# Kernel optimization log

Hardware: AMD Instinct MI355X
Metric: run time of the kernel (lower is better)

The kernel has to match this reference:

```python
import jax, jax.numpy as jnp
import numpy as np

HID = 768          # args.hidden_size
LSTM2 = 768        # args.lstm_dim * 2
SCALE = HID ** -0.5


def _cross_attn(q_in, kv_in, Wq, bq, Wk, bk, Wv, bv):
    # Linear projections (weights stored as [in, out])
    Q = q_in @ Wq + bq            # [B, Sq, H]
    K = kv_in @ Wk + bk           # [B, Sk, H]
    V = kv_in @ Wv + bv           # [B, Sk, H]
    attn = jnp.einsum('bqh,bkh->bqk', Q, K) * SCALE
    attn = jax.nn.softmax(attn, axis=-1)
    return jnp.einsum('bqk,bkh->bqh', attn, V)


def setup_inputs() -> dict:
    key = jax.random.key(0)
    ks = jax.random.split(key, 14)
    B, Ssyn, Ssem = 4, 4096, 2048
    syntactic_feat = jax.random.normal(ks[0], (B, Ssyn, LSTM2), jnp.float32)
    semantic_feat = jax.random.normal(ks[1], (B, Ssem, HID), jnp.float32)

    def lin(k, fan_in, fan_out):
        kw, kb = jax.random.split(k)
        bound = 1.0 / np.sqrt(fan_in)
        W = jax.random.uniform(kw, (fan_in, fan_out), jnp.float32, -bound, bound)
        b = jax.random.uniform(kb, (fan_out,), jnp.float32, -bound, bound)
        return W, b

    # syntax_to_semantic: query_dim=HID, key_dim=LSTM2
    Wq1, bq1 = lin(ks[2], HID, HID)
    Wk1, bk1 = lin(ks[3], LSTM2, HID)
    Wv1, bv1 = lin(ks[4], LSTM2, HID)
    # semantic_to_syntax: query_dim=LSTM2, key_dim=HID
    Wq2, bq2 = lin(ks[5], LSTM2, HID)
    Wk2, bk2 = lin(ks[6], HID, HID)
    Wv2, bv2 = lin(ks[7], HID, HID)
    return dict(syntactic_feat=syntactic_feat, semantic_feat=semantic_feat,
                Wq1=Wq1, bq1=bq1, Wk1=Wk1, bk1=bk1, Wv1=Wv1, bv1=bv1,
                Wq2=Wq2, bq2=bq2, Wk2=Wk2, bk2=bk2, Wv2=Wv2, bv2=bv2)


def reference(syntactic_feat, semantic_feat,
              Wq1, bq1, Wk1, bk1, Wv1, bv1,
              Wq2, bq2, Wk2, bk2, Wv2, bv2):
    # enhanced_semantic: queries from semantic, keys/values from syntactic
    enhanced_semantic = _cross_attn(semantic_feat, syntactic_feat,
                                    Wq1, bq1, Wk1, bk1, Wv1, bv1)
    # enhanced_syntax: queries from syntactic, keys/values from semantic
    enhanced_syntax = _cross_attn(syntactic_feat, semantic_feat,
                                  Wq2, bq2, Wk2, bk2, Wv2, bv2)
    return enhanced_semantic, enhanced_syntax
```

## Files before the change

kernel.cpp:

```cpp
#include <hip/hip_runtime.h>
#include <stdint.h>


typedef unsigned short u16;
typedef __attribute__((ext_vector_type(8))) __bf16 bf16x8;
typedef __attribute__((ext_vector_type(4))) float f32x4;

__device__ __forceinline__ float bf2f(u16 u) {
  union { unsigned int i; float f; } x; x.i = ((unsigned int)u) << 16; return x.f;
}
__device__ __forceinline__ u16 f2bf(float f) {
  union { float f; unsigned int i; } x; x.f = f;
  unsigned int i = x.i;
  i += 0x7fffu + ((i >> 16) & 1u);
  return (u16)(i >> 16);
}

__device__ __forceinline__ void cp16(void* lds, const void* g) {
  __builtin_amdgcn_global_load_lds((__attribute__((address_space(1))) void*)g,
                                   (__attribute__((address_space(3))) void*)lds,
                                   16, 0, 0);
}

struct GemmDesc {
  const u16* A; const u16* Bt; const float* bias; void* C;
  long sA, sB, sC;
  int K, lda, ldb, ldc;
  int gx, gy;
  int start;
  int mode, outf;
  float scale;
};
struct GemmPack { GemmDesc d[6]; int nd; };

#define PHASE(MH, I0, PAR, RDB, STAGE, WAITC)                                 \
  {                                                                           \
    const bf16x8* As8 =                                                       \
        (const bf16x8*)((const char*)L + (PAR) * 32768 + (MH) * 16384);       \
    bf16x8 a0[2][2];                                                          \
    _Pragma("unroll")                                                         \
    for (int s = 0; s < 2; ++s)                                               \
      _Pragma("unroll")                                                       \
      for (int i = 0; i < 2; ++i) a0[s][i] = As8[iaq[s][(I0) + i]];           \
    if (RDB) {                                                                \
      const bf16x8* Bl8 =                                                     \
          (const bf16x8*)((const char*)L + 65536 + (PAR) * 32768);            \
      const bf16x8* Bh8 =                                                     \
          (const bf16x8*)((const char*)L + 65536 + (PAR) * 32768 + 16384);    \
      _Pragma("unroll")                                                       \
      for (int s = 0; s < 2; ++s)                                             \
        _Pragma("unroll")                                                     \
        for (int j = 0; j < 2; ++j) {                                         \
          bfr[0][s][j] = Bl8[ibq[s][j]];                                      \
          bfr[1][s][j] = Bh8[ibq[s][j]];                                      \
        }                                                                     \
    }                                                                         \
    STAGE;                                                                    \
    if (RDB) { asm volatile("s_waitcnt lgkmcnt(8)" ::: "memory"); }           \
    __builtin_amdgcn_s_barrier();                                             \
    asm volatile("s_waitcnt lgkmcnt(0)" ::: "memory");                        \
    __builtin_amdgcn_s_setprio(1);                                            \
    _Pragma("unroll")                                                         \
    for (int s = 0; s < 2; ++s)                                               \
      _Pragma("unroll")                                                       \
      for (int i = 0; i < 2; ++i)                                             \
        _Pragma("unroll")                                                     \
        for (int nh = 0; nh < 2; ++nh)                                        \
          _Pragma("unroll")                                                   \
          for (int j = 0; j < 2; ++j)                                         \
            acc[MH][nh][(I0) + i][j] =                                        \
                __builtin_amdgcn_mfma_f32_16x16x32_bf16(                      \
                    bfr[nh][s][j], a0[s][i], acc[MH][nh][(I0) + i][j],        \
                    0, 0, 0);                                                 \
    __builtin_amdgcn_s_setprio(0);                                            \
    WAITC;                                                                    \
    __builtin_amdgcn_s_barrier();                                             \
  }

__global__ __launch_bounds__(512, 2)
void gemm256_kernel(GemmPack p)
{
  __shared__ __align__(16) u16 L[65536];

  int seg = 0;
#pragma unroll
  for (int t = 1; t < 6; ++t)
    if (t < p.nd && (int)blockIdx.x >= p.d[t].start) seg = t;
  const GemmDesc& g = p.d[seg];
  const int local = (int)blockIdx.x - g.start;
  const int pxy = g.gx * g.gy;
  const int bz = local / pxy;
  const int rem = local - bz * pxy;
  const int by = rem / g.gx;
  const int bx = rem - by * g.gx;

  const int tid  = threadIdx.x;
  const int lane = tid & 63;
  const int wave = tid >> 6;
  const int l15  = lane & 15;
  const int quad = lane >> 4;
  const int wm   = wave >> 2;
  const int wn   = wave & 3;

  const char* Ab = (const char*)(g.A + (long)bz * g.sA + (long)bx * 256 * g.lda);
  const char* Bb = (const char*)(g.Bt + (long)bz * g.sB + (long)by * 256 * g.ldb);
  const long ldaB = (long)g.lda * 2;
  const long ldbB = (long)g.ldb * 2;

  const int gchk = (lane & 7) ^ (lane >> 3);
  const char* pa0 = Ab + (long)(wave * 8 + (lane >> 3)) * ldaB + (gchk << 4);
  const char* pb0 = Bb + (long)(wave * 8 + (lane >> 3)) * ldbB + (gchk << 4);
  char* lA = (char*)L + wave * 1024;
  char* lB = (char*)L + 65536 + wave * 1024;

  auto stA = [&](int tile, int h) {
    char* d = lA + (tile & 1) * 32768 + h * 16384;
    const char* s = pa0 + (long)h * 128 * ldaB + ((long)tile << 7);
    cp16(d, s);
    cp16(d + 8192, s + 64 * ldaB);
  };
  auto stB = [&](int tile, int h) {
    char* d = lB + (tile & 1) * 32768 + h * 16384;
    const char* s = pb0 + (long)h * 128 * ldbB + ((long)tile << 7);
    cp16(d, s);
    cp16(d + 8192, s + 64 * ldbB);
  };

  int iaq[2][4], ibq[2][2];
#pragma unroll
  for (int s = 0; s < 2; ++s) {
#pragma unroll
    for (int i = 0; i < 4; ++i)
      iaq[s][i] = (wm * 64 + i * 16 + l15) * 8 + ((s * 4 + quad) ^ (l15 & 7));
#pragma unroll
    for (int j = 0; j < 2; ++j)
      ibq[s][j] = (wn * 32 + j * 16 + l15) * 8 + ((s * 4 + quad) ^ (l15 & 7));
  }

  f32x4 acc[2][2][4][2];
  {
    f32x4 zz = {0.f, 0.f, 0.f, 0.f};
#pragma unroll
    for (int mh = 0; mh < 2; ++mh)
#pragma unroll
      for (int nh = 0; nh < 2; ++nh)
#pragma unroll
        for (int i = 0; i < 4; ++i)
#pragma unroll
          for (int j = 0; j < 2; ++j) acc[mh][nh][i][j] = zz;
  }
  bf16x8 bfr[2][2][2];

  stB(0, 0); stB(0, 1); stA(0, 0); stA(0, 1);
  stB(1, 0); stB(1, 1); stA(1, 0);
  asm volatile("s_waitcnt vmcnt(6)" ::: "memory");
  __builtin_amdgcn_s_barrier();

  const int nt = g.K >> 6;
  const int NI = nt >> 1;
  for (int it = 0; it < NI; ++it) {
    const int t = it * 2;
    const bool m2 = (t + 2) < nt;
    const bool m3 = (t + 3) < nt;
    PHASE(0, 0, 0, 1, stA(t + 1, 1), )
    PHASE(0, 2, 0, 0, if (m2) stB(t + 2, 0), )
    PHASE(1, 0, 0, 0, if (m2) stB(t + 2, 1), )
    PHASE(1, 2, 0, 0, if (m2) stA(t + 2, 0),
          if (m2) { asm volatile("s_waitcnt vmcnt(6)" ::: "memory"); }
          else    { asm volatile("s_waitcnt vmcnt(0)" ::: "memory"); })
    PHASE(0, 0, 1, 1, if (m2) stA(t + 2, 1), )
    PHASE(0, 2, 1, 0, if (m3) stB(t + 3, 0), )
    PHASE(1, 0, 1, 0, if (m3) stB(t + 3, 1), )
    PHASE(1, 2, 1, 0, if (m3) stA(t + 3, 0),
          if (m3)      { asm volatile("s_waitcnt vmcnt(6)" ::: "memory"); }
          else if (m2) { asm volatile("s_waitcnt vmcnt(0)" ::: "memory"); })
  }

  const long cbase = (long)bz * g.sC;
#pragma unroll
  for (int mh = 0; mh < 2; ++mh) {
#pragma unroll
    for (int i = 0; i < 4; ++i) {
      const int row = bx * 256 + mh * 128 + wm * 64 + i * 16 + l15;
      const float rbias = (g.mode == 2) ? g.bias[row] : 0.f;
#pragma unroll
      for (int nh = 0; nh < 2; ++nh) {
#pragma unroll
        for (int j = 0; j < 2; ++j) {
          const int colbase = by * 256 + nh * 128 + wn * 32 + j * 16 + quad * 4;
          float v[4];
#pragma unroll
          for (int r = 0; r < 4; ++r) v[r] = acc[mh][nh][i][j][r] * g.scale;
          if (g.mode == 1) {
            const float4 cb = *(const float4*)(g.bias + colbase);
            v[0] += cb.x; v[1] += cb.y; v[2] += cb.z; v[3] += cb.w;
          } else if (g.mode == 2) {
#pragma unroll
            for (int r = 0; r < 4; ++r) v[r] += rbias;
          }
          const long idx = cbase + (long)row * g.ldc + colbase;
          if (g.outf) {
            float4 st; st.x = v[0]; st.y = v[1]; st.z = v[2]; st.w = v[3];
            *(float4*)((float*)g.C + idx) = st;
          } else {
            uint2 st;
            st.x = (unsigned int)f2bf(v[0]) | ((unsigned int)f2bf(v[1]) << 16);
            st.y = (unsigned int)f2bf(v[2]) | ((unsigned int)f2bf(v[3]) << 16);
            *(uint2*)((u16*)g.C + idx) = st;
          }
        }
      }
    }
  }
}

__global__ __launch_bounds__(256)
void cvt2_bf16_kernel(const float* __restrict__ sa, u16* __restrict__ da, int n8a,
                      const float* __restrict__ sb, u16* __restrict__ db, int n8b)
{
  int idx = blockIdx.x * 256 + threadIdx.x;
  const float* src; u16* dst; int i;
  if (idx < n8a) { src = sa; dst = da; i = idx; }
  else           { src = sb; dst = db; i = idx - n8a; if (i >= n8b) return; }
  const float4* s4 = (const float4*)src;
  float4 a = s4[i * 2], b = s4[i * 2 + 1];
  uint4 o;
  o.x = (unsigned int)f2bf(a.x) | ((unsigned int)f2bf(a.y) << 16);
  o.y = (unsigned int)f2bf(a.z) | ((unsigned int)f2bf(a.w) << 16);
  o.z = (unsigned int)f2bf(b.x) | ((unsigned int)f2bf(b.y) << 16);
  o.w = (unsigned int)f2bf(b.z) | ((unsigned int)f2bf(b.w) << 16);
  ((uint4*)dst)[i] = o;
}

__global__ void transpose6_kernel(const float* s0, const float* s1, const float* s2,
                                  const float* s3, const float* s4, const float* s5,
                                  u16* d0, u16* d1, u16* d2,
                                  u16* d3, u16* d4, u16* d5)
{
  __shared__ float t[32][33];
  const float* src; u16* dst;
  switch (blockIdx.z) {
    case 0: src = s0; dst = d0; break;
    case 1: src = s1; dst = d1; break;
    case 2: src = s2; dst = d2; break;
    case 3: src = s3; dst = d3; break;
    case 4: src = s4; dst = d4; break;
    default: src = s5; dst = d5; break;
  }
  const int tx = threadIdx.x, ty = threadIdx.y;
  const int x = blockIdx.x * 32 + tx;
  const int y0 = blockIdx.y * 32;
#pragma unroll
  for (int j = 0; j < 32; j += 8) t[ty + j][tx] = src[(long)(y0 + ty + j) * 768 + x];
  __syncthreads();
  const int x2 = y0 + tx;
#pragma unroll
  for (int j = 0; j < 32; j += 8)
    dst[(long)(blockIdx.x * 32 + ty + j) * 768 + x2] = f2bf(t[tx][ty + j]);
}

template <int NV>
__device__ __forceinline__ void softmax_row(u16* row)
{
  __shared__ float red[8];
  const int tid  = threadIdx.x;
  const int lane = tid & 63;
  const int wave = tid >> 6;
  uint4* p4 = (uint4*)row;

  uint4 ld[NV / 8];
#pragma unroll
  for (int c = 0; c < NV / 8; ++c) ld[c] = p4[tid + c * 256];
  float v[NV];
#pragma unroll
  for (int c = 0; c < NV / 8; ++c) {
    unsigned int w[4] = {ld[c].x, ld[c].y, ld[c].z, ld[c].w};
#pragma unroll
    for (int q = 0; q < 4; ++q) {
      v[c * 8 + q * 2]     = bf2f((u16)(w[q] & 0xffffu));
      v[c * 8 + q * 2 + 1] = bf2f((u16)(w[q] >> 16));
    }
  }

  float m = -1e30f;
#pragma unroll
  for (int i = 0; i < NV; ++i) m = fmaxf(m, v[i]);
#pragma unroll
  for (int off = 32; off > 0; off >>= 1) m = fmaxf(m, __shfl_xor(m, off, 64));
  if (lane == 0) red[wave] = m;
  __syncthreads();
  m = fmaxf(fmaxf(red[0], red[1]), fmaxf(red[2], red[3]));

  float s = 0.f;
#pragma unroll
  for (int i = 0; i < NV; ++i) { v[i] = __expf(v[i] - m); s += v[i]; }
#pragma unroll
  for (int off = 32; off > 0; off >>= 1) s += __shfl_xor(s, off, 64);
  if (lane == 0) red[4 + wave] = s;
  __syncthreads();
  s = (red[4] + red[5]) + (red[6] + red[7]);
  const float inv = 1.0f / s;

#pragma unroll
  for (int c = 0; c < NV / 8; ++c) {
    unsigned int w[4];
#pragma unroll
    for (int q = 0; q < 4; ++q) {
      const u16 lo = f2bf(v[c * 8 + q * 2] * inv);
      const u16 hi = f2bf(v[c * 8 + q * 2 + 1] * inv);
      w[q] = (unsigned int)lo | ((unsigned int)hi << 16);
    }
    uint4 st; st.x = w[0]; st.y = w[1]; st.z = w[2]; st.w = w[3];
    p4[tid + c * 256] = st;
  }
}

__global__ __launch_bounds__(256)
void softmax_both_kernel(u16* S1, u16* S2, const u16* cpy_src, u16* cpy_dst)
{
  if (blockIdx.x < 8192) { softmax_row<16>(S1 + (long)blockIdx.x * 4096); return; }
  if (blockIdx.x < 24576) { softmax_row<8>(S2 + (long)(blockIdx.x - 8192) * 2048); return; }
  const long base = (long)(blockIdx.x - 24576) * 512 + threadIdx.x;
  const uint4* s = (const uint4*)cpy_src;
  uint4* d = (uint4*)cpy_dst;
  d[base] = s[base];
  d[base + 256] = s[base + 256];
}


static GemmDesc mkdesc(const void* A, const void* Bt, const float* bias, void* C,
                       long sA, long sB, long sC, int K, int lda, int ldb, int ldc,
                       int M, int N, int start, int mode, int outf, float scale)
{
  GemmDesc d;
  d.A = (const u16*)A; d.Bt = (const u16*)Bt; d.bias = bias; d.C = C;
  d.sA = sA; d.sB = sB; d.sC = sC;
  d.K = K; d.lda = lda; d.ldb = ldb; d.ldc = ldc;
  d.gx = M / 256; d.gy = N / 256; d.start = start;
  d.mode = mode; d.outf = outf; d.scale = scale;
  return d;
}

extern "C" void kernel_launch(void* const* d_in, const int* in_sizes, int n_in,
                              void* d_out, int out_size, void* d_ws, size_t ws_size,
                              hipStream_t stream)
{
  (void)in_sizes; (void)n_in; (void)out_size; (void)ws_size;
  const float* syn = (const float*)d_in[0];
  const float* sem = (const float*)d_in[1];
  const float* W[6]    = {(const float*)d_in[2], (const float*)d_in[4],  (const float*)d_in[6],
                          (const float*)d_in[8], (const float*)d_in[10], (const float*)d_in[12]};
  const float* bias[6] = {(const float*)d_in[3], (const float*)d_in[5],  (const float*)d_in[7],
                          (const float*)d_in[9], (const float*)d_in[11], (const float*)d_in[13]};
  float* out = (float*)d_out;

  u16* ws   = (u16*)d_ws;
  u16* S1   = ws;
  u16* synb = ws;
  u16* semb = ws + 12582912;
  u16* WT   = ws + 18874368;
  u16* S2   = ws + 33554432;
  u16* V1T  = ws + 67108864;
  u16* Q1   = ws + 79691776;
  u16* V2Tc = ws + 79691776;
  u16* K1  = (u16*)out;
  u16* o1  = (u16*)(out + 6291456);
  u16* Q2  = o1;
  u16* K2  = o1 + 12582912;
  u16* V2T = o1 + 18874368;

  const float SC = 0.036084391824351615f;

  cvt2_bf16_kernel<<<dim3(9216), dim3(256), 0, stream>>>(
      syn, synb, 1572864, sem, semb, 786432);

  transpose6_kernel<<<dim3(24, 24, 6), dim3(32, 8, 1), 0, stream>>>(
      W[0], W[1], W[2], W[3], W[4], W[5],
      WT + 0 * 589824, WT + 1 * 589824, WT + 2 * 589824,
      WT + 3 * 589824, WT + 4 * 589824, WT + 5 * 589824);

  {
    GemmPack p; p.nd = 6;
    p.d[0] = mkdesc(synb, WT + 1 * 589824, bias[1], K1, 0, 0, 0,
                    768, 768, 768, 768, 16384, 768, 0, 1, 0, 1.f);
    p.d[1] = mkdesc(synb, WT + 3 * 589824, bias[3], Q2, 0, 0, 0,
                    768, 768, 768, 768, 16384, 768, 192, 1, 0, 1.f);
    p.d[2] = mkdesc(WT + 2 * 589824, synb, bias[2], V1T, 0, 0, 0,
                    768, 768, 768, 16384, 768, 16384, 384, 2, 0, 1.f);
    p.d[3] = mkdesc(semb, WT + 0 * 589824, bias[0], Q1, 0, 0, 0,
                    768, 768, 768, 768, 8192, 768, 576, 1, 0, 1.f);
    p.d[4] = mkdesc(semb, WT + 4 * 589824, bias[4], K2, 0, 0, 0,
                    768, 768, 768, 768, 8192, 768, 672, 1, 0, 1.f);
    p.d[5] = mkdesc(WT + 5 * 589824, semb, bias[5], V2T, 0, 0, 0,
                    768, 768, 768, 8192, 768, 8192, 768, 2, 0, 1.f);
    gemm256_kernel<<<dim3(864), dim3(512), 0, stream>>>(p);
  }

  {
    GemmPack p; p.nd = 2;
    p.d[0] = mkdesc(Q1, K1, nullptr, S1,
                    1572864L, 3145728L, 8388608L,
                    768, 768, 768, 4096, 2048, 4096, 0, 0, 0, SC);
    p.d[1] = mkdesc(Q2, K2, nullptr, S2,
                    3145728L, 1572864L, 8388608L,
                    768, 768, 768, 2048, 4096, 2048, 512, 0, 0, SC);
    gemm256_kernel<<<dim3(1024), dim3(512), 0, stream>>>(p);
  }

  softmax_both_kernel<<<dim3(26112), dim3(256), 0, stream>>>(S1, S2, V2T, V2Tc);

  {
    GemmPack p; p.nd = 2;
    p.d[0] = mkdesc(S1, V1T, nullptr, out,
                    8388608L, 4096L, 1572864L,
                    4096, 4096, 16384, 768, 2048, 768, 0, 0, 1, 1.f);
    p.d[1] = mkdesc(S2, V2Tc, nullptr, out + 6291456,
                    8388608L, 2048L, 3145728L,
                    2048, 2048, 8192, 768, 4096, 768, 96, 0, 1, 1.f);
    gemm256_kernel<<<dim3(288), dim3(512), 0, stream>>>(p);
  }
}
```

Baseline: 566.3 us.

## Remap GEMM block order across XCDs and fuse input conversion with weight transpose

Every GEMM segment now permutes its local block index so that round-robin dispatch (blockIdx mod 8) gives each XCD a contiguous run of output tiles. This should improve L2 reuse of the shared A and B panels. Separately, the fp32-to-bf16 input conversion and the six weight transposes are merged into one launch to save a kernel launch and let the two jobs overlap. The remap assumes each segment's block count and start offset are multiples of 8.

```diff
diff --git a/kernel.cpp b/kernel.cpp
--- a/kernel.cpp
+++ b/kernel.cpp
@@ -27,7 +27,7 @@
   long sA, sB, sC;
   int K, lda, ldb, ldc;
   int gx, gy;
-  int start;
+  int start, nblk;
   int mode, outf;
   float scale;
 };
@@ -87,7 +87,8 @@
   for (int t = 1; t < 6; ++t)
     if (t < p.nd && (int)blockIdx.x >= p.d[t].start) seg = t;
   const GemmDesc& g = p.d[seg];
-  const int local = (int)blockIdx.x - g.start;
+  const int local0 = (int)blockIdx.x - g.start;
+  const int local = (local0 & 7) * (g.nblk >> 3) + (local0 >> 3);
   const int pxy = g.gx * g.gy;
   const int bz = local / pxy;
   const int rem = local - bz * pxy;
@@ -215,48 +216,54 @@
 }
 
 __global__ __launch_bounds__(256)
-void cvt2_bf16_kernel(const float* __restrict__ sa, u16* __restrict__ da, int n8a,
-                      const float* __restrict__ sb, u16* __restrict__ db, int n8b)
-{
-  int idx = blockIdx.x * 256 + threadIdx.x;
-  const float* src; u16* dst; int i;
-  if (idx < n8a) { src = sa; dst = da; i = idx; }
-  else           { src = sb; dst = db; i = idx - n8a; if (i >= n8b) return; }
-  const float4* s4 = (const float4*)src;
-  float4 a = s4[i * 2], b = s4[i * 2 + 1];
-  uint4 o;
-  o.x = (unsigned int)f2bf(a.x) | ((unsigned int)f2bf(a.y) << 16);
-  o.y = (unsigned int)f2bf(a.z) | ((unsigned int)f2bf(a.w) << 16);
-  o.z = (unsigned int)f2bf(b.x) | ((unsigned int)f2bf(b.y) << 16);
-  o.w = (unsigned int)f2bf(b.z) | ((unsigned int)f2bf(b.w) << 16);
-  ((uint4*)dst)[i] = o;
-}
-
-__global__ void transpose6_kernel(const float* s0, const float* s1, const float* s2,
-                                  const float* s3, const float* s4, const float* s5,
-                                  u16* d0, u16* d1, u16* d2,
-                                  u16* d3, u16* d4, u16* d5)
+void prep_kernel(const float* __restrict__ sa, u16* __restrict__ da, int n8a,
+                 const float* __restrict__ sb, u16* __restrict__ db, int n8b,
+                 const float* w0, const float* w1, const float* w2,
+                 const float* w3, const float* w4, const float* w5,
+                 u16* t0, u16* t1, u16* t2, u16* t3, u16* t4, u16* t5)
 {
   __shared__ float t[32][33];
+  const int b = blockIdx.x;
+  const int tid = threadIdx.x;
+  if (b < 9216) {
+    int idx = b * 256 + tid;
+    const float* src; u16* dst; int i;
+    if (idx < n8a) { src = sa; dst = da; i = idx; }
+    else           { src = sb; dst = db; i = idx - n8a; if (i >= n8b) return; }
+    const float4* s4 = (const float4*)src;
+    float4 a = s4[i * 2], c = s4[i * 2 + 1];
+    uint4 o;
+    o.x = (unsigned int)f2bf(a.x) | ((unsigned int)f2bf(a.y) << 16);
+    o.y = (unsigned int)f2bf(a.z) | ((unsigned int)f2bf(a.w) << 16);
+    o.z = (unsigned int)f2bf(c.x) | ((unsigned int)f2bf(c.y) << 16);
+    o.w = (unsigned int)f2bf(c.z) | ((unsigned int)f2bf(c.w) << 16);
+    ((uint4*)dst)[i] = o;
+    return;
+  }
+  const int tb = b - 9216;
+  const int z  = tb / 576;
+  const int r  = tb - z * 576;
+  const int byy = r / 24;
+  const int bxx = r - byy * 24;
   const float* src; u16* dst;
-  switch (blockIdx.z) {
-    case 0: src = s0; dst = d0; break;
-    case 1: src = s1; dst = d1; break;
-    case 2: src = s2; dst = d2; break;
-    case 3: src = s3; dst = d3; break;
-    case 4: src = s4; dst = d4; break;
-    default: src = s5; dst = d5; break;
-  }
-  const int tx = threadIdx.x, ty = threadIdx.y;
-  const int x = blockIdx.x * 32 + tx;
-  const int y0 = blockIdx.y * 32;
+  switch (z) {
+    case 0: src = w0; dst = t0; break;
+    case 1: src = w1; dst = t1; break;
+    case 2: src = w2; dst = t2; break;
+    case 3: src = w3; dst = t3; break;
+    case 4: src = w4; dst = t4; break;
+    default: src = w5; dst = t5; break;
+  }
+  const int tx = tid & 31, ty = tid >> 5;
+  const int x = bxx * 32 + tx;
+  const int y0 = byy * 32;
 #pragma unroll
   for (int j = 0; j < 32; j += 8) t[ty + j][tx] = src[(long)(y0 + ty + j) * 768 + x];
   __syncthreads();
   const int x2 = y0 + tx;
 #pragma unroll
   for (int j = 0; j < 32; j += 8)
-    dst[(long)(blockIdx.x * 32 + ty + j) * 768 + x2] = f2bf(t[tx][ty + j]);
+    dst[(long)(bxx * 32 + ty + j) * 768 + x2] = f2bf(t[tx][ty + j]);
 }
 
 template <int NV>
@@ -330,13 +337,15 @@
 
 static GemmDesc mkdesc(const void* A, const void* Bt, const float* bias, void* C,
                        long sA, long sB, long sC, int K, int lda, int ldb, int ldc,
-                       int M, int N, int start, int mode, int outf, float scale)
+                       int M, int N, int nb, int start, int mode, int outf,
+                       float scale)
 {
   GemmDesc d;
   d.A = (const u16*)A; d.Bt = (const u16*)Bt; d.bias = bias; d.C = C;
   d.sA = sA; d.sB = sB; d.sC = sC;
   d.K = K; d.lda = lda; d.ldb = ldb; d.ldc = ldc;
   d.gx = M / 256; d.gy = N / 256; d.start = start;
+  d.nblk = nb * d.gx * d.gy;
   d.mode = mode; d.outf = outf; d.scale = scale;
   return d;
 }
@@ -371,10 +380,8 @@
 
   const float SC = 0.036084391824351615f;
 
-  cvt2_bf16_kernel<<<dim3(9216), dim3(256), 0, stream>>>(
-      syn, synb, 1572864, sem, semb, 786432);
-
-  transpose6_kernel<<<dim3(24, 24, 6), dim3(32, 8, 1), 0, stream>>>(
+  prep_kernel<<<dim3(12672), dim3(256), 0, stream>>>(
+      syn, synb, 1572864, sem, semb, 786432,
       W[0], W[1], W[2], W[3], W[4], W[5],
       WT + 0 * 589824, WT + 1 * 589824, WT + 2 * 589824,
       WT + 3 * 589824, WT + 4 * 589824, WT + 5 * 589824);
@@ -382,17 +389,17 @@
   {
     GemmPack p; p.nd = 6;
     p.d[0] = mkdesc(synb, WT + 1 * 589824, bias[1], K1, 0, 0, 0,
-                    768, 768, 768, 768, 16384, 768, 0, 1, 0, 1.f);
+                    768, 768, 768, 768, 16384, 768, 1, 0, 1, 0, 1.f);
     p.d[1] = mkdesc(synb, WT + 3 * 589824, bias[3], Q2, 0, 0, 0,
-                    768, 768, 768, 768, 16384, 768, 192, 1, 0, 1.f);
+                    768, 768, 768, 768, 16384, 768, 1, 192, 1, 0, 1.f);
     p.d[2] = mkdesc(WT + 2 * 589824, synb, bias[2], V1T, 0, 0, 0,
-                    768, 768, 768, 16384, 768, 16384, 384, 2, 0, 1.f);
+                    768, 768, 768, 16384, 768, 16384, 1, 384, 2, 0, 1.f);
     p.d[3] = mkdesc(semb, WT + 0 * 589824, bias[0], Q1, 0, 0, 0,
-                    768, 768, 768, 768, 8192, 768, 576, 1, 0, 1.f);
+                    768, 768, 768, 768, 8192, 768, 1, 576, 1, 0, 1.f);
     p.d[4] = mkdesc(semb, WT + 4 * 589824, bias[4], K2, 0, 0, 0,
-                    768, 768, 768, 768, 8192, 768, 672, 1, 0, 1.f);
+                    768, 768, 768, 768, 8192, 768, 1, 672, 1, 0, 1.f);
     p.d[5] = mkdesc(WT + 5 * 589824, semb, bias[5], V2T, 0, 0, 0,
-                    768, 768, 768, 8192, 768, 8192, 768, 2, 0, 1.f);
+                    768, 768, 768, 8192, 768, 8192, 1, 768, 2, 0, 1.f);
     gemm256_kernel<<<dim3(864), dim3(512), 0, stream>>>(p);
   }
 
@@ -400,10 +407,10 @@
     GemmPack p; p.nd = 2;
     p.d[0] = mkdesc(Q1, K1, nullptr, S1,
                     1572864L, 3145728L, 8388608L,
-                    768, 768, 768, 4096, 2048, 4096, 0, 0, 0, SC);
+                    768, 768, 768, 4096, 2048, 4096, 4, 0, 0, 0, SC);
     p.d[1] = mkdesc(Q2, K2, nullptr, S2,
                     3145728L, 1572864L, 8388608L,
-                    768, 768, 768, 2048, 4096, 2048, 512, 0, 0, SC);
+                    768, 768, 768, 2048, 4096, 2048, 4, 512, 0, 0, SC);
     gemm256_kernel<<<dim3(1024), dim3(512), 0, stream>>>(p);
   }
 
@@ -413,10 +420,10 @@
     GemmPack p; p.nd = 2;
     p.d[0] = mkdesc(S1, V1T, nullptr, out,
                     8388608L, 4096L, 1572864L,
-                    4096, 4096, 16384, 768, 2048, 768, 0, 0, 1, 1.f);
+                    4096, 4096, 16384, 768, 2048, 768, 4, 0, 0, 1, 1.f);
     p.d[1] = mkdesc(S2, V2Tc, nullptr, out + 6291456,
                     8388608L, 2048L, 3145728L,
-                    2048, 2048, 8192, 768, 4096, 768, 96, 0, 1, 1.f);
+                    2048, 2048, 8192, 768, 4096, 768, 4, 96, 0, 1, 1.f);
     gemm256_kernel<<<dim3(288), dim3(512), 0, stream>>>(p);
   }
 }
```

Result: no change. 566.8 us (+0.1%).
